# Optimization experiments

Measured on AMD Instinct MI355X. Metric: run time of the kernel, lower is better.

Reference implementation:

```python
import jax, jax.numpy as jnp
import numpy as np

N, M, D = 8192, 8192, 256

def setup_inputs() -> dict:
    key = jax.random.key(0)
    k1, k2 = jax.random.split(key)
    fmap1 = jax.random.normal(k1, (N, D), dtype=jnp.float32)
    fmap2 = jax.random.normal(k2, (M, D), dtype=jnp.float32)
    return {"fmap1": fmap1, "fmap2": fmap2}

def reference(fmap1, fmap2):
    # corr[n, m] = <fmap1[n], fmap2[m]> / sqrt(D), then row-wise softmax
    scale = fmap1.shape[-1] ** 0.5
    corr = jnp.einsum('nd,md->nm', fmap1, fmap2) / scale
    return jax.nn.softmax(corr, axis=-1)
```

## Files before the change

### kernel.cpp

```cpp
#include <hip/hip_runtime.h>
#include <stddef.h>

typedef _Float16 half8 __attribute__((ext_vector_type(8)));
typedef float floatx4 __attribute__((ext_vector_type(4)));
typedef float float4v __attribute__((ext_vector_type(4)));

#define NR 8192
#define MC 8192
#define KD 256
#define BM 128
#define BN 128
#define BK 64
#define LOGIT_SCALE 0.0625f

__global__ void convert_kernel(const float* __restrict__ f1, const float* __restrict__ f2,
                               _Float16* __restrict__ h1, _Float16* __restrict__ h2,
                               float* __restrict__ rowsum) {
    int t = blockIdx.x * 256 + threadIdx.x;
    if (blockIdx.x < 32) rowsum[blockIdx.x * 256 + threadIdx.x] = 0.0f;
    int arr = t >> 18;
    int idx = (t & 262143) * 8;
    const float* src = arr ? f2 : f1;
    _Float16* dst = arr ? h2 : h1;
    float4v a = *(const float4v*)(src + idx);
    float4v b = *(const float4v*)(src + idx + 4);
    half8 h;
    h[0] = (_Float16)a[0]; h[1] = (_Float16)a[1];
    h[2] = (_Float16)a[2]; h[3] = (_Float16)a[3];
    h[4] = (_Float16)b[0]; h[5] = (_Float16)b[1];
    h[6] = (_Float16)b[2]; h[7] = (_Float16)b[3];
    *(half8*)(dst + idx) = h;
}

template <int MODE>
__launch_bounds__(256, 3)
__global__ void corr_gemm(const _Float16* __restrict__ A, const _Float16* __restrict__ B,
                          float* __restrict__ rowsum, float* __restrict__ out) {
    __shared__ __align__(16) _Float16 As[BM * BK];
    __shared__ __align__(16) _Float16 Bs[BM * BK];

    const int tid  = threadIdx.x;
    const int lane = tid & 63;
    const int wid  = tid >> 6;
    const int wr   = wid >> 1;
    const int wc   = wid & 1;

    int bid = blockIdx.x;
    int swz = (bid & 7) * 512 + (bid >> 3);
    int tn = (swz >> 9) * 8 + (swz & 7);
    int tm = (swz & 511) >> 3;

    const _Float16* Abase = A + (size_t)(tm * BM) * KD;
    const _Float16* Bbase = B + (size_t)(tn * BN) * KD;

    floatx4 acc[4][4];
#pragma unroll
    for (int i = 0; i < 4; ++i)
#pragma unroll
        for (int j = 0; j < 4; ++j) acc[i][j] = floatx4{0.f, 0.f, 0.f, 0.f};

#pragma unroll
    for (int kt = 0; kt < 4; ++kt) {
#pragma unroll
        for (int m = 0; m < 2; ++m) {
            const _Float16* src = m ? Bbase : Abase;
            _Float16* lbase = m ? &Bs[0] : &As[0];
#pragma unroll
            for (int i = 0; i < 4; ++i) {
                int L = i * 256 + tid;
                int row  = L >> 3;
                int slot = L & 7;
                const _Float16* g = src + row * KD + kt * BK + slot * 8;
                _Float16* l = lbase + (size_t)(i * 256 + wid * 64) * 8;
                __builtin_amdgcn_global_load_lds(
                    (const __attribute__((address_space(1))) void*)g,
                    (__attribute__((address_space(3))) void*)l, 16, 0, 0);
            }
        }
        __syncthreads();

#pragma unroll
        for (int kc = 0; kc < 2; ++kc) {
            half8 af[4], bf[4];
#pragma unroll
            for (int f = 0; f < 4; ++f) {
                int rowA = wr * 64 + f * 16 + (lane & 15);
                int ks   = kc * 4 + (lane >> 4);
                af[f] = *(const half8*)(&As[rowA * BK + ks * 8]);
                int rowB = wc * 64 + f * 16 + (lane & 15);
                bf[f] = *(const half8*)(&Bs[rowB * BK + ks * 8]);
            }
#pragma unroll
            for (int i = 0; i < 4; ++i)
#pragma unroll
                for (int j = 0; j < 4; ++j)
                    acc[i][j] = __builtin_amdgcn_mfma_f32_16x16x32_f16(af[i], bf[j], acc[i][j], 0, 0, 0);
        }
        __syncthreads();
    }

    if (MODE == 0) {
#pragma unroll
        for (int i = 0; i < 4; ++i) {
#pragma unroll
            for (int r = 0; r < 4; ++r) {
                float s = 0.f;
#pragma unroll
                for (int j = 0; j < 4; ++j) s += __expf(acc[i][j][r] * LOGIT_SCALE);
                s += __shfl_xor(s, 1);
                s += __shfl_xor(s, 2);
                s += __shfl_xor(s, 4);
                s += __shfl_xor(s, 8);
                if ((lane & 15) == 0) {
                    int row = tm * BM + wr * 64 + i * 16 + (lane >> 4) * 4 + r;
                    atomicAdd(&rowsum[row], s);
                }
            }
        }
    } else {
#pragma unroll
        for (int i = 0; i < 4; ++i) {
#pragma unroll
            for (int r = 0; r < 4; ++r) {
                int row = tm * BM + wr * 64 + i * 16 + (lane >> 4) * 4 + r;
                float rinv = 1.0f / rowsum[row];
                float* orow = out + (size_t)row * MC + tn * BN + wc * 64 + (lane & 15);
#pragma unroll
                for (int j = 0; j < 4; ++j)
                    orow[j * 16] = __expf(acc[i][j][r] * LOGIT_SCALE) * rinv;
            }
        }
    }
}

extern "C" void kernel_launch(void* const* d_in, const int* in_sizes, int n_in,
                              void* d_out, int out_size, void* d_ws, size_t ws_size,
                              hipStream_t stream) {
    const float* f1 = (const float*)d_in[0];
    const float* f2 = (const float*)d_in[1];
    float* out = (float*)d_out;

    _Float16* h1 = (_Float16*)d_ws;
    _Float16* h2 = h1 + (size_t)NR * KD;
    float* rowsum = (float*)(h2 + (size_t)MC * KD);

    convert_kernel<<<2048, 256, 0, stream>>>(f1, f2, h1, h2, rowsum);
    corr_gemm<0><<<4096, 256, 0, stream>>>(h1, h2, rowsum, nullptr);
    corr_gemm<1><<<4096, 256, 0, stream>>>(h1, h2, rowsum, out);
}
```

Measured before the change: 385.4 us.

## Double-buffer K halves in LDS with XOR-swizzled layout to overlap loads

```diff
diff --git a/kernel.cpp b/kernel.cpp
--- a/kernel.cpp
+++ b/kernel.cpp
@@ -10,7 +10,7 @@
 #define KD 256
 #define BM 128
 #define BN 128
-#define BK 64
+#define KH 128
 #define LOGIT_SCALE 0.0625f
 
 __global__ void convert_kernel(const float* __restrict__ f1, const float* __restrict__ f2,
@@ -33,11 +33,11 @@
 }
 
 template <int MODE>
-__launch_bounds__(256, 3)
+__launch_bounds__(256, 1)
 __global__ void corr_gemm(const _Float16* __restrict__ A, const _Float16* __restrict__ B,
                           float* __restrict__ rowsum, float* __restrict__ out) {
-    __shared__ __align__(16) _Float16 As[BM * BK];
-    __shared__ __align__(16) _Float16 Bs[BM * BK];
+    __shared__ __align__(16) _Float16 As[2][BM * KH];
+    __shared__ __align__(16) _Float16 Bs[2][BN * KH];
 
     const int tid  = threadIdx.x;
     const int lane = tid & 63;
@@ -53,42 +53,45 @@
     const _Float16* Abase = A + (size_t)(tm * BM) * KD;
     const _Float16* Bbase = B + (size_t)(tn * BN) * KD;
 
+    auto stage = [&](int h) {
+#pragma unroll
+        for (int m = 0; m < 2; ++m) {
+            const _Float16* src = m ? Bbase : Abase;
+            _Float16* lbase = m ? &Bs[h][0] : &As[h][0];
+#pragma unroll
+            for (int i = 0; i < 8; ++i) {
+                int L = i * 256 + tid;
+                int row   = L >> 4;
+                int pslot = L & 15;
+                int kslot = (pslot & 8) | ((pslot ^ row) & 7);
+                const _Float16* g = src + row * KD + h * KH + kslot * 8;
+                _Float16* l = lbase + (size_t)(i * 256 + wid * 64) * 8;
+                __builtin_amdgcn_global_load_lds(
+                    (const __attribute__((address_space(1))) void*)g,
+                    (__attribute__((address_space(3))) void*)l, 16, 0, 0);
+            }
+        }
+    };
+
     floatx4 acc[4][4];
 #pragma unroll
     for (int i = 0; i < 4; ++i)
 #pragma unroll
         for (int j = 0; j < 4; ++j) acc[i][j] = floatx4{0.f, 0.f, 0.f, 0.f};
 
+    auto compute = [&](int h) {
 #pragma unroll
-    for (int kt = 0; kt < 4; ++kt) {
-#pragma unroll
-        for (int m = 0; m < 2; ++m) {
-            const _Float16* src = m ? Bbase : Abase;
-            _Float16* lbase = m ? &Bs[0] : &As[0];
-#pragma unroll
-            for (int i = 0; i < 4; ++i) {
-                int L = i * 256 + tid;
-                int row  = L >> 3;
-                int slot = L & 7;
-                const _Float16* g = src + row * KD + kt * BK + slot * 8;
-                _Float16* l = lbase + (size_t)(i * 256 + wid * 64) * 8;
-                __builtin_amdgcn_global_load_lds(
-                    (const __attribute__((address_space(1))) void*)g,
-                    (__attribute__((address_space(3))) void*)l, 16, 0, 0);
-            }
-        }
-        __syncthreads();
-
-#pragma unroll
-        for (int kc = 0; kc < 2; ++kc) {
+        for (int kc = 0; kc < 4; ++kc) {
             half8 af[4], bf[4];
+            int ks = kc * 4 + (lane >> 4);
 #pragma unroll
             for (int f = 0; f < 4; ++f) {
                 int rowA = wr * 64 + f * 16 + (lane & 15);
-                int ks   = kc * 4 + (lane >> 4);
-                af[f] = *(const half8*)(&As[rowA * BK + ks * 8]);
+                int psA  = (ks & 8) | ((ks ^ rowA) & 7);
+                af[f] = *(const half8*)(&As[h][rowA * KH + psA * 8]);
                 int rowB = wc * 64 + f * 16 + (lane & 15);
-                bf[f] = *(const half8*)(&Bs[rowB * BK + ks * 8]);
+                int psB  = (ks & 8) | ((ks ^ rowB) & 7);
+                bf[f] = *(const half8*)(&Bs[h][rowB * KH + psB * 8]);
             }
 #pragma unroll
             for (int i = 0; i < 4; ++i)
@@ -96,8 +99,14 @@
                 for (int j = 0; j < 4; ++j)
                     acc[i][j] = __builtin_amdgcn_mfma_f32_16x16x32_f16(af[i], bf[j], acc[i][j], 0, 0, 0);
         }
-        __syncthreads();
-    }
+    };
+
+    stage(0);
+    __syncthreads();
+    stage(1);
+    compute(0);
+    __syncthreads();
+    compute(1);
 
     if (MODE == 0) {
 #pragma unroll
```

Result: slower. 466.2 us (+21.0%).
